# Performance work log

Measured on AMD Instinct MI355X. Metric: run time of the kernel, lower is better.

## Reference

```python
import jax, jax.numpy as jnp
import numpy as np

N = 100000
E = 600000
NODE_DIM = 128
EDGE_DIM = 32
HIDDEN = 128  # must equal NODE_DIM (index_add_ into zeros_like(node_features))


def _linear_params(key, fan_in, fan_out):
    kw, kb = jax.random.split(key)
    bound = 1.0 / np.sqrt(fan_in)
    W = jax.random.uniform(kw, (fan_in, fan_out), minval=-bound, maxval=bound, dtype=jnp.float32)
    b = jax.random.uniform(kb, (fan_out,), minval=-bound, maxval=bound, dtype=jnp.float32)
    return W, b


def setup_inputs() -> dict:
    key = jax.random.key(0)
    ks = jax.random.split(key, 8)
    node_features = jax.random.normal(ks[0], (N, NODE_DIM), dtype=jnp.float32)
    edge_index = jax.random.randint(ks[1], (2, E), 0, N, dtype=jnp.int32)
    edge_features = jax.random.normal(ks[2], (E, EDGE_DIM), dtype=jnp.float32)
    m_W1, m_b1 = _linear_params(ks[3], 2 * NODE_DIM + EDGE_DIM, HIDDEN)
    m_W2, m_b2 = _linear_params(ks[4], HIDDEN, HIDDEN)
    a_W, a_b = _linear_params(ks[5], HIDDEN, 1)
    u_W1, u_b1 = _linear_params(ks[6], NODE_DIM + HIDDEN, HIDDEN)
    u_W2, u_b2 = _linear_params(ks[7], HIDDEN, NODE_DIM)
    return {
        "node_features": node_features,
        "edge_features": edge_features,
        "m_W1": m_W1, "m_b1": m_b1, "m_W2": m_W2, "m_b2": m_b2,
        "a_W": a_W, "a_b": a_b,
        "u_W1": u_W1, "u_b1": u_b1, "u_W2": u_W2, "u_b2": u_b2,
        "edge_index": edge_index,
    }


def reference(node_features, edge_features, m_W1, m_b1, m_W2, m_b2,
              a_W, a_b, u_W1, u_b1, u_W2, u_b2, edge_index):
    row, col = edge_index[0], edge_index[1]
    # gather endpoints + edge feats -> [E, 2*node_dim + edge_dim]
    msg_in = jnp.concatenate([node_features[row], node_features[col], edge_features], axis=-1)
    # message MLP
    h = jax.nn.relu(msg_in @ m_W1 + m_b1)
    messages = h @ m_W2 + m_b2  # [E, hidden]
    # global softmax over all edges (dim=0), per attention column (width 1)
    attn = jax.nn.softmax(messages @ a_W + a_b, axis=0)  # [E, 1]
    messages = messages * attn
    # scatter-add into destination nodes
    aggregated = jax.ops.segment_sum(messages, col, num_segments=node_features.shape[0])
    # update MLP + residual
    upd_in = jnp.concatenate([node_features, aggregated], axis=-1)
    u = jax.nn.relu(upd_in @ u_W1 + u_b1)
    updated = u @ u_W2 + u_b2
    return updated + node_features
```

## Files before the change

### kernel.cpp

```cpp
#include <hip/hip_runtime.h>
#include <hip/hip_bf16.h>
#include <hip/hip_fp8.h>
#include <stdint.h>

#define NN 100000
#define NE 600000
#define ND 128
#define ED 32
#define HID 128
#define SCANB 391
#define NEB 4688

using short8 = __attribute__((ext_vector_type(8))) short;
using f32x4  = __attribute__((ext_vector_type(4))) float;
using f32x2  = __attribute__((ext_vector_type(2))) float;

__device__ __forceinline__ uint32_t f2bf(float f) {
  uint32_t u = __float_as_uint(f);
  return (u + 0x7FFFu + ((u >> 16) & 1u)) >> 16;
}
__device__ __forceinline__ float bf2f(uint32_t h) {
  return __uint_as_float(h << 16);
}
__device__ __forceinline__ short8 pack8(float4 a, float4 b) {
  short8 s;
  s[0] = (short)f2bf(a.x); s[1] = (short)f2bf(a.y);
  s[2] = (short)f2bf(a.z); s[3] = (short)f2bf(a.w);
  s[4] = (short)f2bf(b.x); s[5] = (short)f2bf(b.y);
  s[6] = (short)f2bf(b.z); s[7] = (short)f2bf(b.w);
  return s;
}

__device__ __forceinline__ uint8_t fp8_enc(float v) {
#if __has_builtin(__builtin_amdgcn_cvt_pk_fp8_f32)
  return (uint8_t)(__builtin_amdgcn_cvt_pk_fp8_f32(v, v, 0, false) & 0xFF);
#else
  __hip_fp8_e4m3 q(v);
  return q.__x;
#endif
}
__device__ __forceinline__ float2 fp8_dec2(uint32_t v) {
#if __has_builtin(__builtin_amdgcn_cvt_pk_f32_fp8)
  f32x2 r = __builtin_amdgcn_cvt_pk_f32_fp8((int)v, false);
  return make_float2(r[0], r[1]);
#else
  __hip_fp8_e4m3 qa, qb;
  qa.__x = (uint8_t)(v & 0xFF); qb.__x = (uint8_t)((v >> 8) & 0xFF);
  return make_float2((float)qa, (float)qb);
#endif
}

__global__ __launch_bounds__(256) void k_prep_all(
    const float* __restrict__ uW1, const float* __restrict__ uW2,
    const float* __restrict__ W1, const float* __restrict__ W2,
    short* __restrict__ U1p, short* __restrict__ U2p,
    uint8_t* __restrict__ W1p8, uint8_t* __restrict__ W2p8) {
  int o = blockIdx.x * 256 + threadIdx.x;
  const float* src; int rel; int isFp8;
  short* dstS = nullptr; uint8_t* dst8 = nullptr;
  if (o < 32768)       { rel = o;         src = uW1; dstS = U1p;  isFp8 = 0; }
  else if (o < 49152)  { rel = o - 32768; src = uW2; dstS = U2p;  isFp8 = 0; }
  else if (o < 86016)  { rel = o - 49152; src = W1;  dst8 = W1p8; isFp8 = 1; }
  else if (o < 102400) { rel = o - 86016; src = W2;  dst8 = W2p8; isFp8 = 1; }
  else return;
  int j = rel & 7, c16 = (rel >> 3) & 15, g = (rel >> 7) & 3, nt = (rel >> 9) & 7, c = rel >> 12;
  int k = c * 32 + g * 8 + j, n = nt * 16 + c16;
  float v = src[k * 128 + n];
  if (isFp8) dst8[rel] = fp8_enc(v);
  else       dstS[rel] = (short)f2bf(v);
}

__global__ __launch_bounds__(256) void k_prep_nf(const float* __restrict__ nf,
                                                 short* __restrict__ nfb,
                                                 uint8_t* __restrict__ nfb8,
                                                 int* __restrict__ cnt) {
  const int total = NN * ND / 8;
  int gid = blockIdx.x * 256 + threadIdx.x;
  for (int i = gid; i < NN; i += gridDim.x * 256) cnt[i] = 0;
  for (int u = gid; u < total; u += gridDim.x * 256) {
    const float* s = nf + (size_t)u * 8;
    float4 v0 = *(const float4*)s, v1 = *(const float4*)(s + 4);
    *(short8*)(nfb + (size_t)u * 8) = pack8(v0, v1);
    uint8_t b[8];
    b[0] = fp8_enc(v0.x); b[1] = fp8_enc(v0.y); b[2] = fp8_enc(v0.z); b[3] = fp8_enc(v0.w);
    b[4] = fp8_enc(v1.x); b[5] = fp8_enc(v1.y); b[6] = fp8_enc(v1.z); b[7] = fp8_enc(v1.w);
    *(uint2*)(nfb8 + (size_t)u * 8) = *(const uint2*)b;
  }
}

__global__ __launch_bounds__(256, 3) void k_edge_mfma(
    const uint8_t* __restrict__ nfb8, const float* __restrict__ ef,
    const uint8_t* __restrict__ W1p8, const float* __restrict__ b1,
    const uint8_t* __restrict__ W2p8, const float* __restrict__ b2,
    const float* __restrict__ aW, const int* __restrict__ ei,
    const int* __restrict__ perm,
    uint8_t* __restrict__ msg8, float* __restrict__ logits) {
  __shared__ __align__(16) uint8_t sRow[128 * 136];
  __shared__ __align__(16) uint8_t sCol[128 * 136];
  __shared__ __align__(16) uint8_t sEf[128 * 40];
  __shared__ __align__(16) uint8_t sB8[2][4096];
  __shared__ int sIdx[256];
  __shared__ int sPerm[128];

  const int tid = threadIdx.x;
  const int wv = tid >> 6, ln = tid & 63, cr = ln & 15, gp = ln >> 4;
  const int e0 = blockIdx.x * 128;
  const int wrow = wv * 32;

  if (tid < 128) {
    int e = e0 + tid; if (e >= NE) e = NE - 1;
    sIdx[tid] = ei[e];
    sIdx[128 + tid] = ei[NE + e];
    sPerm[tid] = perm[e];
  }
  __syncthreads();

#pragma unroll
  for (int it = 0; it < 16; ++it) {
    int t = it * 256 + tid;
    int side = t >> 11;
    int r = (t & 2047) >> 4;
    int o = (t & 15) * 8;
    const uint8_t* src = nfb8 + (size_t)sIdx[side * 128 + r] * ND + o;
    uint8_t* dst = (side ? sCol : sRow) + r * 136 + o;
    *(uint2*)dst = *(const uint2*)src;
  }
#pragma unroll
  for (int it = 0; it < 2; ++it) {
    int u = it * 256 + tid;
    int r = u >> 2, o = (u & 3) * 8;
    int e = e0 + r; if (e >= NE) e = NE - 1;
    const float* src = ef + (size_t)e * ED + o;
    float4 v0 = *(const float4*)src, v1 = *(const float4*)(src + 4);
    uint8_t b[8];
    b[0] = fp8_enc(v0.x); b[1] = fp8_enc(v0.y); b[2] = fp8_enc(v0.z); b[3] = fp8_enc(v0.w);
    b[4] = fp8_enc(v1.x); b[5] = fp8_enc(v1.y); b[6] = fp8_enc(v1.z); b[7] = fp8_enc(v1.w);
    *(uint2*)&sEf[r * 40 + o] = *(const uint2*)b;
  }
  *(uint4*)&sB8[0][tid * 16] = *(const uint4*)(W1p8 + tid * 16);

  float bia[8], aWr[8], bia2[8];
#pragma unroll
  for (int nt = 0; nt < 8; ++nt) {
    bia[nt] = b1[nt * 16 + cr];
    bia2[nt] = b2[nt * 16 + cr];
    aWr[nt] = aW[nt * 16 + cr];
  }
  f32x4 acc[2][8];
#pragma unroll
  for (int mt = 0; mt < 2; ++mt)
#pragma unroll
    for (int nt = 0; nt < 8; ++nt)
      acc[mt][nt] = (f32x4){bia[nt], bia[nt], bia[nt], bia[nt]};
  __syncthreads();

  for (int c = 0; c < 9; ++c) {
    if (c < 8)
      *(uint4*)&sB8[(c + 1) & 1][tid * 16] =
          *(const uint4*)(W1p8 + (c + 1) * 4096 + tid * 16);
    const uint8_t* aSrc = (c < 4) ? (sRow + c * 32)
                        : (c < 8) ? (sCol + (c - 4) * 32) : sEf;
    const int pitch = (c == 8) ? 40 : 136;
    long af0 = *(const long*)(aSrc + (wrow + cr) * pitch + gp * 8);
    long af1 = *(const long*)(aSrc + (wrow + 16 + cr) * pitch + gp * 8);
    const uint8_t* bbuf = sB8[c & 1];
#pragma unroll
    for (int nt = 0; nt < 8; ++nt) {
      long bfr = *(const long*)&bbuf[(nt * 4 + gp) * 128 + cr * 8];
      acc[0][nt] = __builtin_amdgcn_mfma_f32_16x16x32_fp8_fp8(af0, bfr, acc[0][nt], 0, 0, 0);
      acc[1][nt] = __builtin_amdgcn_mfma_f32_16x16x32_fp8_fp8(af1, bfr, acc[1][nt], 0, 0, 0);
    }
    __syncthreads();
  }

#pragma unroll
  for (int mt = 0; mt < 2; ++mt)
#pragma unroll
    for (int nt = 0; nt < 8; ++nt)
#pragma unroll
      for (int rr = 0; rr < 4; ++rr)
        sRow[(wrow + mt * 16 + gp * 4 + rr) * 136 + nt * 16 + cr] =
            fp8_enc(fmaxf(acc[mt][nt][rr], 0.f));
  *(uint4*)&sB8[0][tid * 16] = *(const uint4*)(W2p8 + tid * 16);
  __syncthreads();

  f32x4 acc2[2][8];
#pragma unroll
  for (int mt = 0; mt < 2; ++mt)
#pragma unroll
    for (int nt = 0; nt < 8; ++nt)
      acc2[mt][nt] = (f32x4){bia2[nt], bia2[nt], bia2[nt], bia2[nt]};
  for (int c2 = 0; c2 < 4; ++c2) {
    if (c2 < 3)
      *(uint4*)&sB8[(c2 + 1) & 1][tid * 16] =
          *(const uint4*)(W2p8 + (c2 + 1) * 4096 + tid * 16);
    long af0 = *(const long*)&sRow[(wrow + cr) * 136 + c2 * 32 + gp * 8];
    long af1 = *(const long*)&sRow[(wrow + 16 + cr) * 136 + c2 * 32 + gp * 8];
    const uint8_t* bbuf = sB8[c2 & 1];
#pragma unroll
    for (int nt = 0; nt < 8; ++nt) {
      long bfr = *(const long*)&bbuf[(nt * 4 + gp) * 128 + cr * 8];
      acc2[0][nt] = __builtin_amdgcn_mfma_f32_16x16x32_fp8_fp8(af0, bfr, acc2[0][nt], 0, 0, 0);
      acc2[1][nt] = __builtin_amdgcn_mfma_f32_16x16x32_fp8_fp8(af1, bfr, acc2[1][nt], 0, 0, 0);
    }
    __syncthreads();
  }

#pragma unroll
  for (int mt = 0; mt < 2; ++mt)
#pragma unroll
    for (int rr = 0; rr < 4; ++rr) {
      float p = 0.f;
#pragma unroll
      for (int nt = 0; nt < 8; ++nt) p += acc2[mt][nt][rr] * aWr[nt];
      p += __shfl_xor(p, 1, 64);
      p += __shfl_xor(p, 2, 64);
      p += __shfl_xor(p, 4, 64);
      p += __shfl_xor(p, 8, 64);
      int row = wrow + mt * 16 + gp * 4 + rr;
      if (cr == 0 && e0 + row < NE) logits[sPerm[row]] = p;
    }

#pragma unroll
  for (int mt = 0; mt < 2; ++mt)
#pragma unroll
    for (int nt = 0; nt < 8; ++nt)
#pragma unroll
      for (int rr = 0; rr < 4; ++rr)
        sCol[(wrow + mt * 16 + gp * 4 + rr) * 136 + nt * 16 + cr] =
            fp8_enc(acc2[mt][nt][rr]);
  __syncthreads();
#pragma unroll
  for (int it = 0; it < 8; ++it) {
    int row = it * 16 + (tid >> 4), o8 = (tid & 15) * 8;
    if (e0 + row < NE)
      *(uint2*)(msg8 + (size_t)sPerm[row] * HID + o8) = *(const uint2*)&sCol[row * 136 + o8];
  }
}

__global__ __launch_bounds__(256, 2) void k_node_mfma(
    const short* __restrict__ nfb, const short* __restrict__ aggb,
    const short* __restrict__ U1p, const float* __restrict__ b1,
    const short* __restrict__ U2p, const float* __restrict__ b2,
    float* __restrict__ out) {
  __shared__ __align__(16) short sA[192 * 40];
  __shared__ __align__(16) short sB[4096];
  __shared__ __align__(16) short sH[192 * 136];

  const int tid = threadIdx.x;
  const int wv = tid >> 6, ln = tid & 63, cr = ln & 15, gp = ln >> 4;
  const int n0 = blockIdx.x * 192;
  const int wrow = wv * 48;

  float bia[8], bia2[8];
#pragma unroll
  for (int nt = 0; nt < 8; ++nt) {
    bia[nt] = b1[nt * 16 + cr];
    bia2[nt] = b2[nt * 16 + cr];
  }
  f32x4 acc[3][8];
#pragma unroll
  for (int mt = 0; mt < 3; ++mt)
#pragma unroll
    for (int nt = 0; nt < 8; ++nt)
      acc[mt][nt] = (f32x4){bia[nt], bia[nt], bia[nt], bia[nt]};

  for (int c = 0; c < 8; ++c) {
#pragma unroll
    for (int it = 0; it < 3; ++it) {
      int row = it * 64 + (tid >> 2), k8 = (tid & 3) * 8;
      int n = n0 + row; if (n >= NN) n = NN - 1;
      const short* src = (c < 4) ? nfb + (size_t)n * ND + c * 32 + k8
                                 : aggb + (size_t)n * ND + (c - 4) * 32 + k8;
      *(short8*)&sA[row * 40 + k8] = *(const short8*)src;
    }
    {
      const short8* wsrc = (const short8*)(U1p + c * 4096);
      short8 t0 = wsrc[tid], t1 = wsrc[tid + 256];
      ((short8*)sB)[tid] = t0; ((short8*)sB)[tid + 256] = t1;
    }
    __syncthreads();
    short8 af[3];
#pragma unroll
    for (int mt = 0; mt < 3; ++mt)
      af[mt] = *(const short8*)&sA[(wrow + mt * 16 + cr) * 40 + gp * 8];
#pragma unroll
    for (int nt = 0; nt < 8; ++nt) {
      short8 bfr = *(const short8*)&sB[(nt * 4 + gp) * 128 + cr * 8];
#pragma unroll
      for (int mt = 0; mt < 3; ++mt)
        acc[mt][nt] = __builtin_amdgcn_mfma_f32_16x16x32_bf16(af[mt], bfr, acc[mt][nt], 0, 0, 0);
    }
    __syncthreads();
  }

#pragma unroll
  for (int mt = 0; mt < 3; ++mt)
#pragma unroll
    for (int nt = 0; nt < 8; ++nt)
#pragma unroll
      for (int rr = 0; rr < 4; ++rr)
        sH[(wrow + mt * 16 + gp * 4 + rr) * 136 + nt * 16 + cr] =
            (short)f2bf(fmaxf(acc[mt][nt][rr], 0.f));
  __syncthreads();

  f32x4 acc2[3][8];
#pragma unroll
  for (int mt = 0; mt < 3; ++mt)
#pragma unroll
    for (int nt = 0; nt < 8; ++nt)
      acc2[mt][nt] = (f32x4){bia2[nt], bia2[nt], bia2[nt], bia2[nt]};
  for (int c2 = 0; c2 < 4; ++c2) {
    {
      const short8* wsrc = (const short8*)(U2p + c2 * 4096);
      short8 t0 = wsrc[tid], t1 = wsrc[tid + 256];
      ((short8*)sB)[tid] = t0; ((short8*)sB)[tid + 256] = t1;
    }
    __syncthreads();
    short8 af[3];
#pragma unroll
    for (int mt = 0; mt < 3; ++mt)
      af[mt] = *(const short8*)&sH[(wrow + mt * 16 + cr) * 136 + c2 * 32 + gp * 8];
#pragma unroll
    for (int nt = 0; nt < 8; ++nt) {
      short8 bfr = *(const short8*)&sB[(nt * 4 + gp) * 128 + cr * 8];
#pragma unroll
      for (int mt = 0; mt < 3; ++mt)
        acc2[mt][nt] = __builtin_amdgcn_mfma_f32_16x16x32_bf16(af[mt], bfr, acc2[mt][nt], 0, 0, 0);
    }
    __syncthreads();
  }

#pragma unroll
  for (int mt = 0; mt < 3; ++mt)
#pragma unroll
    for (int rr = 0; rr < 4; ++rr) {
      int n = n0 + wrow + mt * 16 + gp * 4 + rr;
      if (n < NN) {
#pragma unroll
        for (int nt = 0; nt < 8; ++nt) {
          int col = nt * 16 + cr;
          float r = bf2f((uint16_t)nfb[(size_t)n * ND + col]);
          out[(size_t)n * ND + col] = acc2[mt][nt][rr] + r;
        }
      }
    }
}

__device__ __forceinline__ void ms_combine(float& m, float& s, float m2, float s2) {
  float M = fmaxf(m, m2);
  s = s * expf(m - M) + s2 * expf(m2 - M);
  m = M;
}
__device__ __forceinline__ void ms_block_reduce(float& m, float& s) {
#pragma unroll
  for (int o = 1; o < 64; o <<= 1) {
    float m2 = __shfl_xor(m, o, 64), s2 = __shfl_xor(s, o, 64);
    ms_combine(m, s, m2, s2);
  }
  __shared__ float sm[4], ss[4];
  if ((threadIdx.x & 63) == 0) { sm[threadIdx.x >> 6] = m; ss[threadIdx.x >> 6] = s; }
  __syncthreads();
  m = sm[0]; s = ss[0];
  ms_combine(m, s, sm[1], ss[1]);
  ms_combine(m, s, sm[2], ss[2]);
  ms_combine(m, s, sm[3], ss[3]);
}
__global__ __launch_bounds__(256) void k_red_p(const float* __restrict__ logits,
                                               float* __restrict__ pmax,
                                               float* __restrict__ psum) {
  float m = -3.402823466e38f, s = 0.f;
  for (int i = blockIdx.x * 256 + threadIdx.x; i < NE; i += 1024 * 256) {
    float l = logits[i];
    if (l <= m) s += expf(l - m);
    else { s = s * expf(m - l) + 1.f; m = l; }
  }
  ms_block_reduce(m, s);
  if (threadIdx.x == 0) { pmax[blockIdx.x] = m; psum[blockIdx.x] = s; }
}
__global__ __launch_bounds__(256) void k_red_f(const float* __restrict__ pmax,
                                               const float* __restrict__ psum,
                                               float* __restrict__ red) {
  float m = pmax[threadIdx.x], s = psum[threadIdx.x];
  ms_combine(m, s, pmax[threadIdx.x + 256], psum[threadIdx.x + 256]);
  ms_combine(m, s, pmax[threadIdx.x + 512], psum[threadIdx.x + 512]);
  ms_combine(m, s, pmax[threadIdx.x + 768], psum[threadIdx.x + 768]);
  ms_block_reduce(m, s);
  if (threadIdx.x == 0) { red[0] = m; red[1] = 1.0f / s; }
}

__global__ __launch_bounds__(256) void k_hist(const int* __restrict__ ei,
                                              int* __restrict__ cnt) {
  int e = blockIdx.x * 256 + threadIdx.x;
  if (e < NE) atomicAdd(&cnt[ei[NE + e]], 1);
}
__global__ __launch_bounds__(256) void k_scan_bsum(const int* __restrict__ cnt,
                                                   int* __restrict__ bsum) {
  int i = blockIdx.x * 256 + threadIdx.x;
  int v = (i < NN) ? cnt[i] : 0;
#pragma unroll
  for (int s = 1; s < 64; s <<= 1) v += __shfl_xor(v, s, 64);
  __shared__ int sv[4];
  if ((threadIdx.x & 63) == 0) sv[threadIdx.x >> 6] = v;
  __syncthreads();
  if (threadIdx.x == 0) bsum[blockIdx.x] = sv[0] + sv[1] + sv[2] + sv[3];
}
__global__ __launch_bounds__(512) void k_scan_boff(const int* __restrict__ bsum,
                                                   int* __restrict__ boff,
                                                   int* __restrict__ rowptr) {
  __shared__ int s[512];
  int t = threadIdx.x;
  int v = (t < SCANB) ? bsum[t] : 0;
  s[t] = v;
  __syncthreads();
  for (int off = 1; off < 512; off <<= 1) {
    int u = (t >= off) ? s[t - off] : 0;
    __syncthreads();
    s[t] += u;
    __syncthreads();
  }
  if (t < SCANB) boff[t] = s[t] - v;
  if (t == 0) rowptr[NN] = NE;
}
__global__ __launch_bounds__(256) void k_scan_final(int* __restrict__ cnt,
                                                    const int* __restrict__ boff,
                                                    int* __restrict__ rowptr) {
  __shared__ int s[256];
  int b = blockIdx.x, t = threadIdx.x, i = b * 256 + t;
  int v = (i < NN) ? cnt[i] : 0;
  s[t] = v;
  __syncthreads();
  for (int off = 1; off < 256; off <<= 1) {
    int u = (t >= off) ? s[t - off] : 0;
    __syncthreads();
    s[t] += u;
    __syncthreads();
  }
  int excl = s[t] - v + boff[b];
  if (i < NN) { rowptr[i] = excl; cnt[i] = excl; }
}
__global__ __launch_bounds__(256) void k_fill(const int* __restrict__ ei,
                                              int* __restrict__ cursor,
                                              int* __restrict__ perm) {
  int e = blockIdx.x * 256 + threadIdx.x;
  if (e >= NE) return;
  int c = ei[NE + e];
  int pos = atomicAdd(&cursor[c], 1);
  perm[e] = pos;
}

__global__ __launch_bounds__(256) void k_agg(
    const uint8_t* __restrict__ msg8, const float* __restrict__ logits,
    const int* __restrict__ rowptr, const float* __restrict__ red,
    short* __restrict__ aggb) {
  int n = blockIdx.x * 4 + (threadIdx.x >> 6);
  int lane = threadIdx.x & 63;
  if (n >= NN) return;
  float gm = red[0], inv = red[1];
  int i0 = rowptr[n], i1 = rowptr[n + 1];
  float a0 = 0.f, a1 = 0.f;
  for (int i = i0; i < i1; ++i) {
    float wt = expf(logits[i] - gm) * inv;
    uint32_t pk = *(const uint16_t*)(msg8 + (size_t)i * HID + lane * 2);
    float2 d = fp8_dec2(pk);
    a0 += wt * d.x;
    a1 += wt * d.y;
  }
  uint32_t packed = f2bf(a0) | (f2bf(a1) << 16);
  *(uint32_t*)(aggb + (size_t)n * ND + lane * 2) = packed;
}

extern "C" void kernel_launch(void* const* d_in, const int* in_sizes, int n_in,
                              void* d_out, int out_size, void* d_ws, size_t ws_size,
                              hipStream_t stream) {
  const float* nf  = (const float*)d_in[0];
  const float* ef  = (const float*)d_in[1];
  const float* mW1 = (const float*)d_in[2];
  const float* mb1 = (const float*)d_in[3];
  const float* mW2 = (const float*)d_in[4];
  const float* mb2 = (const float*)d_in[5];
  const float* aW  = (const float*)d_in[6];
  const float* uW1 = (const float*)d_in[8];
  const float* ub1 = (const float*)d_in[9];
  const float* uW2 = (const float*)d_in[10];
  const float* ub2 = (const float*)d_in[11];
  const int*   ei  = (const int*)d_in[12];
  float* out = (float*)d_out;

  char* ws = (char*)d_ws;
  uint8_t* msg8 = (uint8_t*)ws;
  float* logits = (float*)(ws + 76800000);
  float* pmax = (float*)(ws + 79200000);
  float* psum = pmax + 1024;
  float* red  = psum + 1024;
  uint8_t* W1p8 = (uint8_t*)(ws + 79208256);
  uint8_t* W2p8 = W1p8 + 36864;
  short* U1p = (short*)(W2p8 + 16384);
  short* U2p = U1p + 32768;
  int* rowptr = (int*)(ws + 79413056);
  int* cnt    = rowptr + (NN + 1);
  int* perm   = cnt + NN;
  int* bsum   = perm + NE;
  int* boff   = bsum + 512;
  short* nfb  = (short*)(ws + 82620000);
  uint8_t* nfb8 = (uint8_t*)(ws + 108220000);
  short* aggb = (short*)(ws + 121020000);

  k_prep_all<<<400, 256, 0, stream>>>(uW1, uW2, mW1, mW2, U1p, U2p, W1p8, W2p8);
  k_prep_nf<<<2048, 256, 0, stream>>>(nf, nfb, nfb8, cnt);
  k_hist<<<(NE + 255) / 256, 256, 0, stream>>>(ei, cnt);
  k_scan_bsum<<<SCANB, 256, 0, stream>>>(cnt, bsum);
  k_scan_boff<<<1, 512, 0, stream>>>(bsum, boff, rowptr);
  k_scan_final<<<SCANB, 256, 0, stream>>>(cnt, boff, rowptr);
  k_fill<<<(NE + 255) / 256, 256, 0, stream>>>(ei, cnt, perm);
  k_edge_mfma<<<NEB, 256, 0, stream>>>(nfb8, ef, W1p8, mb1, W2p8, mb2, aW, ei, perm,
                                       msg8, logits);
  k_red_p<<<1024, 256, 0, stream>>>(logits, pmax, psum);
  k_red_f<<<1, 256, 0, stream>>>(pmax, psum, red);
  k_agg<<<(NN + 3) / 4, 256, 0, stream>>>(msg8, logits, rowptr, red, aggb);
  k_node_mfma<<<(NN + 191) / 192, 256, 0, stream>>>(nfb, aggb, U1p, ub1, U2p, ub2, out);
}
```

Measured before the change: 298.1 us.

## Load node-MLP fragments directly from global memory, drop LDS staging and barriers

The node update kernel no longer stages input rows and weight chunks through shared memory with block-wide barriers. Each wave now loads its A fragments and the weight B fragments straight from global memory (weights are expected to hit in cache), and only the hidden activations go through LDS, which is private per wave so no barrier is needed. The tile shrinks from 192 to 128 rows per block and occupancy is raised to 4 blocks per CU. The aim is to remove the synchronisation and LDS copy overhead, at the cost of redundant weight fetches per wave and uncoalesced fragment loads.

```diff
diff --git a/kernel.cpp b/kernel.cpp
--- a/kernel.cpp
+++ b/kernel.cpp
@@ -238,19 +238,20 @@
   }
 }
 
-__global__ __launch_bounds__(256, 2) void k_node_mfma(
+__global__ __launch_bounds__(256, 4) void k_node_mfma(
     const short* __restrict__ nfb, const short* __restrict__ aggb,
     const short* __restrict__ U1p, const float* __restrict__ b1,
     const short* __restrict__ U2p, const float* __restrict__ b2,
     float* __restrict__ out) {
-  __shared__ __align__(16) short sA[192 * 40];
-  __shared__ __align__(16) short sB[4096];
-  __shared__ __align__(16) short sH[192 * 136];
+  __shared__ __align__(16) short sH[128 * 136];
 
   const int tid = threadIdx.x;
   const int wv = tid >> 6, ln = tid & 63, cr = ln & 15, gp = ln >> 4;
-  const int n0 = blockIdx.x * 192;
-  const int wrow = wv * 48;
+  const int n0 = blockIdx.x * 128;
+  const int wrow = wv * 32;
+
+  int na0 = n0 + wrow + cr;      if (na0 >= NN) na0 = NN - 1;
+  int na1 = n0 + wrow + 16 + cr; if (na1 >= NN) na1 = NN - 1;
 
   float bia[8], bia2[8];
 #pragma unroll
@@ -258,81 +259,58 @@
     bia[nt] = b1[nt * 16 + cr];
     bia2[nt] = b2[nt * 16 + cr];
   }
-  f32x4 acc[3][8];
-#pragma unroll
-  for (int mt = 0; mt < 3; ++mt)
+  f32x4 acc[2][8];
+#pragma unroll
+  for (int mt = 0; mt < 2; ++mt)
 #pragma unroll
     for (int nt = 0; nt < 8; ++nt)
       acc[mt][nt] = (f32x4){bia[nt], bia[nt], bia[nt], bia[nt]};
 
+#pragma unroll
   for (int c = 0; c < 8; ++c) {
-#pragma unroll
-    for (int it = 0; it < 3; ++it) {
-      int row = it * 64 + (tid >> 2), k8 = (tid & 3) * 8;
-      int n = n0 + row; if (n >= NN) n = NN - 1;
-      const short* src = (c < 4) ? nfb + (size_t)n * ND + c * 32 + k8
-                                 : aggb + (size_t)n * ND + (c - 4) * 32 + k8;
-      *(short8*)&sA[row * 40 + k8] = *(const short8*)src;
+    const short* base = (c < 4) ? nfb : aggb;
+    const int ko = (c & 3) * 32 + gp * 8;
+    short8 af0 = *(const short8*)(base + (size_t)na0 * ND + ko);
+    short8 af1 = *(const short8*)(base + (size_t)na1 * ND + ko);
+    const short* Wc = U1p + c * 4096;
+#pragma unroll
+    for (int nt = 0; nt < 8; ++nt) {
+      short8 bfr = *(const short8*)(Wc + (nt * 4 + gp) * 128 + cr * 8);
+      acc[0][nt] = __builtin_amdgcn_mfma_f32_16x16x32_bf16(af0, bfr, acc[0][nt], 0, 0, 0);
+      acc[1][nt] = __builtin_amdgcn_mfma_f32_16x16x32_bf16(af1, bfr, acc[1][nt], 0, 0, 0);
     }
-    {
-      const short8* wsrc = (const short8*)(U1p + c * 4096);
-      short8 t0 = wsrc[tid], t1 = wsrc[tid + 256];
-      ((short8*)sB)[tid] = t0; ((short8*)sB)[tid + 256] = t1;
-    }
-    __syncthreads();
-    short8 af[3];
-#pragma unroll
-    for (int mt = 0; mt < 3; ++mt)
-      af[mt] = *(const short8*)&sA[(wrow + mt * 16 + cr) * 40 + gp * 8];
-#pragma unroll
-    for (int nt = 0; nt < 8; ++nt) {
-      short8 bfr = *(const short8*)&sB[(nt * 4 + gp) * 128 + cr * 8];
-#pragma unroll
-      for (int mt = 0; mt < 3; ++mt)
-        acc[mt][nt] = __builtin_amdgcn_mfma_f32_16x16x32_bf16(af[mt], bfr, acc[mt][nt], 0, 0, 0);
-    }
-    __syncthreads();
-  }
-
-#pragma unroll
-  for (int mt = 0; mt < 3; ++mt)
+  }
+
+#pragma unroll
+  for (int mt = 0; mt < 2; ++mt)
 #pragma unroll
     for (int nt = 0; nt < 8; ++nt)
 #pragma unroll
       for (int rr = 0; rr < 4; ++rr)
         sH[(wrow + mt * 16 + gp * 4 + rr) * 136 + nt * 16 + cr] =
             (short)f2bf(fmaxf(acc[mt][nt][rr], 0.f));
-  __syncthreads();
-
-  f32x4 acc2[3][8];
-#pragma unroll
-  for (int mt = 0; mt < 3; ++mt)
+
+  f32x4 acc2[2][8];
+#pragma unroll
+  for (int mt = 0; mt < 2; ++mt)
 #pragma unroll
     for (int nt = 0; nt < 8; ++nt)
       acc2[mt][nt] = (f32x4){bia2[nt], bia2[nt], bia2[nt], bia2[nt]};
+#pragma unroll
   for (int c2 = 0; c2 < 4; ++c2) {
-    {
-      const short8* wsrc = (const short8*)(U2p + c2 * 4096);
-      short8 t0 = wsrc[tid], t1 = wsrc[tid + 256];
-      ((short8*)sB)[tid] = t0; ((short8*)sB)[tid + 256] = t1;
+    short8 af0 = *(const short8*)&sH[(wrow + cr) * 136 + c2 * 32 + gp * 8];
+    short8 af1 = *(const short8*)&sH[(wrow + 16 + cr) * 136 + c2 * 32 + gp * 8];
+    const short* Wc = U2p + c2 * 4096;
+#pragma unroll
+    for (int nt = 0; nt < 8; ++nt) {
+      short8 bfr = *(const short8*)(Wc + (nt * 4 + gp) * 128 + cr * 8);
+      acc2[0][nt] = __builtin_amdgcn_mfma_f32_16x16x32_bf16(af0, bfr, acc2[0][nt], 0, 0, 0);
+      acc2[1][nt] = __builtin_amdgcn_mfma_f32_16x16x32_bf16(af1, bfr, acc2[1][nt], 0, 0, 0);
     }
-    __syncthreads();
-    short8 af[3];
-#pragma unroll
-    for (int mt = 0; mt < 3; ++mt)
-      af[mt] = *(const short8*)&sH[(wrow + mt * 16 + cr) * 136 + c2 * 32 + gp * 8];
-#pragma unroll
-    for (int nt = 0; nt < 8; ++nt) {
-      short8 bfr = *(const short8*)&sB[(nt * 4 + gp) * 128 + cr * 8];
-#pragma unroll
-      for (int mt = 0; mt < 3; ++mt)
-        acc2[mt][nt] = __builtin_amdgcn_mfma_f32_16x16x32_bf16(af[mt], bfr, acc2[mt][nt], 0, 0, 0);
-    }
-    __syncthreads();
-  }
-
-#pragma unroll
-  for (int mt = 0; mt < 3; ++mt)
+  }
+
+#pragma unroll
+  for (int mt = 0; mt < 2; ++mt)
 #pragma unroll
     for (int rr = 0; rr < 4; ++rr) {
       int n = n0 + wrow + mt * 16 + gp * 4 + rr;
@@ -518,5 +496,5 @@
   k_red_p<<<1024, 256, 0, stream>>>(logits, pmax, psum);
   k_red_f<<<1, 256, 0, stream>>>(pmax, psum, red);
   k_agg<<<(NN + 3) / 4, 256, 0, stream>>>(msg8, logits, rowptr, red, aggb);
-  k_node_mfma<<<(NN + 191) / 192, 256, 0, stream>>>(nfb, aggb, U1p, ub1, U2p, ub2, out);
-}
+  k_node_mfma<<<(NN + 127) / 128, 256, 0, stream>>>(nfb, aggb, U1p, ub1, U2p, ub2, out);
+}
```

Measured after the change: 295.9 us. No clear change (-0.7%).
